# Performance work log

Measured on AMD Instinct MI355X. Metric: run time of the kernel, lower is better.

## Reference

```python
import jax, jax.numpy as jnp
import numpy as np

SIZE = (128, 128, 128)  # volume dims (X, Y, Z)
B, N, C = 2, 2097152, 1


def setup_inputs() -> dict:
    key = jax.random.key(0)
    k1, k2 = jax.random.split(key)
    image = jax.random.normal(k1, (B, SIZE[0], SIZE[1], SIZE[2], C), dtype=jnp.float32)
    grid = jax.random.uniform(k2, (B, N, 3), dtype=jnp.float32)  # normalized coords in [0,1]
    return {"image": image, "grid": grid}


def reference(image, grid):
    # image: [B, X, Y, Z, C]; grid: [B, N, 3] normalized -> trilinear sample -> [B, N, C]
    factor = jnp.array(SIZE, dtype=jnp.float32)
    idx = jnp.clip(grid * factor, 0.001, float(min(SIZE)) - 1.001)  # [B, N, 3]
    x, y, z = idx[..., 0], idx[..., 1], idx[..., 2]
    x1, x2 = jnp.floor(x), jnp.ceil(x)
    y1, y2 = jnp.floor(y), jnp.ceil(y)
    z1, z2 = jnp.floor(z), jnp.ceil(z)

    b = jnp.arange(image.shape[0])[:, None]  # [B, 1] batch index for gathers

    def g(xi, yi, zi):  # corner gather -> [B, N, C]
        return image[b, xi.astype(jnp.int32), yi.astype(jnp.int32), zi.astype(jnp.int32)]

    wx, wx2 = (x - x1)[..., None], (x2 - x)[..., None]
    wy, wy2 = (y - y1)[..., None], (y2 - y)[..., None]
    wz, wz2 = (z - z1)[..., None], (z2 - z)[..., None]

    lerp_y1 = (g(x2, y1, z1) * wx + g(x1, y1, z1) * wx2) * wy2 \
            + (g(x2, y2, z1) * wx + g(x1, y2, z1) * wx2) * wy
    lerp_y2 = (g(x2, y1, z2) * wx + g(x1, y1, z2) * wx2) * wy2 \
            + (g(x2, y2, z2) * wx + g(x1, y2, z2) * wx2) * wy
    return lerp_y2 * wz + lerp_y1 * wz2
```

## Files before the change

### kernel.cpp

```cpp
#include <hip/hip_runtime.h>
#include <hip/hip_fp16.h>


#define TOTAL   (2 * 2097152)
#define LOG2N   21
#define VOL     (128 * 128 * 128)
#define NVOX    (2 * VOL)

__global__ __launch_bounds__(256)
void ImageWarped_cvt_fp16_kernel(const float* __restrict__ in,
                                 __half* __restrict__ out)
{
    const int i = blockIdx.x * 256 + threadIdx.x;
    const float4 v = ((const float4*)in)[i];
    union { __half2 h2[2]; uint2 u; } p;
    p.h2[0] = __floats2half2_rn(v.x, v.y);
    p.h2[1] = __floats2half2_rn(v.z, v.w);
    ((uint2*)out)[i] = p.u;
}

__global__ __launch_bounds__(256)
void ImageWarped_trilinear_h2_kernel(const __half* __restrict__ image,
                                     const float* __restrict__ grid,
                                     float* __restrict__ out)
{
    const int batch = blockIdx.x & 1;
    const int s     = (blockIdx.x >> 1) * 256 + threadIdx.x;
    const int i     = (batch << LOG2N) | s;

    const float gx = grid[3 * i + 0];
    const float gy = grid[3 * i + 1];
    const float gz = grid[3 * i + 2];

    const __half* __restrict__ img = image + ((size_t)batch << LOG2N);

    const float xf = fminf(fmaxf(gx * 128.0f, 0.001f), 126.999f);
    const float yf = fminf(fmaxf(gy * 128.0f, 0.001f), 126.999f);
    const float zf = fminf(fmaxf(gz * 128.0f, 0.001f), 126.999f);

    const float x1f = floorf(xf), x2f = ceilf(xf);
    const float y1f = floorf(yf), y2f = ceilf(yf);
    const float z1f = floorf(zf), z2f = ceilf(zf);

    const float wx  = xf - x1f, wx2 = x2f - xf;
    const float wy  = yf - y1f, wy2 = y2f - yf;
    const float wz  = zf - z1f, wz2 = z2f - zf;

    const int ix1 = (int)x1f, ix2 = (int)x2f;
    const int iy1 = (int)y1f, iy2 = (int)y2f;
    const int iz1 = (int)z1f;

    const int bx1 = ix1 << 14, bx2 = ix2 << 14;
    const int by1 = iy1 << 7,  by2 = iy2 << 7;

    const int ze = min(iz1 & ~1, 124);
    const int sh = (iz1 - ze) << 4;

    const float  ww  = wz2, wwz = wz;
    auto zfetch = [&](int off) -> float {
        const uint2 u = *(const uint2*)(img + off + ze);
        unsigned long long w = ((unsigned long long)u.y << 32) | u.x;
        w >>= sh;
        union { unsigned int u32; __half2 h; } c;
        c.u32 = (unsigned int)w;
        const float2 f = __half22float2(c.h);
        return f.x * ww + f.y * wwz;
    };

    const float q11 = zfetch(bx1 + by1);
    const float q21 = zfetch(bx2 + by1);
    const float q12 = zfetch(bx1 + by2);
    const float q22 = zfetch(bx2 + by2);

    out[i] = (q21 * wx + q11 * wx2) * wy2
           + (q22 * wx + q12 * wx2) * wy;
}

__global__ __launch_bounds__(256)
void ImageWarped_trilinear_f_kernel(const float* __restrict__ image,
                                    const float* __restrict__ grid,
                                    float* __restrict__ out)
{
    const int i = blockIdx.x * 256 + threadIdx.x;
    if (i >= TOTAL) return;

    const float gx = grid[3 * i + 0];
    const float gy = grid[3 * i + 1];
    const float gz = grid[3 * i + 2];

    const int b = i >> LOG2N;
    const float* __restrict__ img = image + (size_t)b * VOL;

    const float xf = fminf(fmaxf(gx * 128.0f, 0.001f), 126.999f);
    const float yf = fminf(fmaxf(gy * 128.0f, 0.001f), 126.999f);
    const float zf = fminf(fmaxf(gz * 128.0f, 0.001f), 126.999f);

    const float x1f = floorf(xf), x2f = ceilf(xf);
    const float y1f = floorf(yf), y2f = ceilf(yf);
    const float z1f = floorf(zf), z2f = ceilf(zf);

    const float wx  = xf - x1f, wx2 = x2f - xf;
    const float wy  = yf - y1f, wy2 = y2f - yf;
    const float wz  = zf - z1f, wz2 = z2f - zf;

    const int ix1 = (int)x1f, ix2 = (int)x2f;
    const int iy1 = (int)y1f, iy2 = (int)y2f;
    const int iz1 = (int)z1f, iz2 = (int)z2f;

    const int bx1 = ix1 << 14, bx2 = ix2 << 14;
    const int by1 = iy1 << 7,  by2 = iy2 << 7;

    const float c111 = img[bx1 + by1 + iz1];
    const float c211 = img[bx2 + by1 + iz1];
    const float c121 = img[bx1 + by2 + iz1];
    const float c221 = img[bx2 + by2 + iz1];
    const float c112 = img[bx1 + by1 + iz2];
    const float c212 = img[bx2 + by1 + iz2];
    const float c122 = img[bx1 + by2 + iz2];
    const float c222 = img[bx2 + by2 + iz2];

    const float lerp_y1 = (c211 * wx + c111 * wx2) * wy2
                        + (c221 * wx + c121 * wx2) * wy;
    const float lerp_y2 = (c212 * wx + c112 * wx2) * wy2
                        + (c222 * wx + c122 * wx2) * wy;

    out[i] = lerp_y2 * wz + lerp_y1 * wz2;
}

extern "C" void kernel_launch(void* const* d_in, const int* in_sizes, int n_in,
                              void* d_out, int out_size, void* d_ws, size_t ws_size,
                              hipStream_t stream)
{
    const float* image = (const float*)d_in[0];
    const float* grid  = (const float*)d_in[1];
    float* out = (float*)d_out;

    const int blocks = (TOTAL + 255) / 256;

    if (ws_size >= (size_t)NVOX * sizeof(__half)) {
        __half* img16 = (__half*)d_ws;
        ImageWarped_cvt_fp16_kernel<<<NVOX / 4 / 256, 256, 0, stream>>>(image, img16);
        ImageWarped_trilinear_h2_kernel<<<blocks, 256, 0, stream>>>(img16, grid, out);
    } else {
        ImageWarped_trilinear_f_kernel<<<blocks, 256, 0, stream>>>(image, grid, out);
    }
}
```

Before: 174.2 us.

## Bin samples by spatial cell and sample from LDS-cached volume tiles

Adds a two-pass scheme. The first kernel sorts each sample into one of 512 16^3 cells per batch using shared-memory histograms and global atomic cursors, and writes the clamped coordinates plus the output index as 16-byte records. The second kernel loads a 17^3 fp32 tile of the volume into LDS for each cell and interpolates every binned sample from that tile. The goal is to replace random global gathers with LDS reads. In exchange it reads the grid twice, writes and reads large record buffers, scatters the output writes, and needs about 84 MB of workspace, falling back to the old paths when that is not available.

```diff
diff --git a/kernel.cpp b/kernel.cpp
--- a/kernel.cpp
+++ b/kernel.cpp
@@ -2,10 +2,173 @@
 #include <hip/hip_fp16.h>
 
 
-#define TOTAL   (2 * 2097152)
-#define LOG2N   21
-#define VOL     (128 * 128 * 128)
-#define NVOX    (2 * VOL)
+#define TOTAL    (2 * 2097152)
+#define LOG2N    21
+#define VOL      (128 * 128 * 128)
+#define NVOX     (2 * VOL)
+#define NCELLS   1024
+#define CAP      5120
+#define SPT      16
+#define TILE_N   (17 * 17 * 18)
+
+typedef unsigned int uint32;
+
+__device__ __forceinline__ float trilerp_direct(const float* __restrict__ img,
+                                                float xf, float yf, float zf)
+{
+    const float x1f = floorf(xf), x2f = ceilf(xf);
+    const float y1f = floorf(yf), y2f = ceilf(yf);
+    const float z1f = floorf(zf), z2f = ceilf(zf);
+    const float wx = xf - x1f, wx2 = x2f - xf;
+    const float wy = yf - y1f, wy2 = y2f - yf;
+    const float wz = zf - z1f, wz2 = z2f - zf;
+    const int bx1 = ((int)x1f) << 14, bx2 = ((int)x2f) << 14;
+    const int by1 = ((int)y1f) << 7,  by2 = ((int)y2f) << 7;
+    const int iz1 = (int)z1f,         iz2 = (int)z2f;
+    const float c111 = img[bx1 + by1 + iz1], c211 = img[bx2 + by1 + iz1];
+    const float c121 = img[bx1 + by2 + iz1], c221 = img[bx2 + by2 + iz1];
+    const float c112 = img[bx1 + by1 + iz2], c212 = img[bx2 + by1 + iz2];
+    const float c122 = img[bx1 + by2 + iz2], c222 = img[bx2 + by2 + iz2];
+    const float l1 = (c211 * wx + c111 * wx2) * wy2 + (c221 * wx + c121 * wx2) * wy;
+    const float l2 = (c212 * wx + c112 * wx2) * wy2 + (c222 * wx + c122 * wx2) * wy;
+    return l2 * wz + l1 * wz2;
+}
+
+__global__ __launch_bounds__(256)
+void ImageWarped_bin_kernel(const float* __restrict__ grid,
+                            const float* __restrict__ image,
+                            float* __restrict__ out,
+                            uint32* __restrict__ cursor,
+                            uint4* __restrict__ records)
+{
+    __shared__ uint32 hist[NCELLS];
+    __shared__ uint32 lbase[NCELLS];
+    __shared__ uint32 rank[NCELLS];
+
+    const int tid = threadIdx.x;
+    for (int b = tid; b < NCELLS; b += 256) { hist[b] = 0; rank[b] = 0; }
+    __syncthreads();
+
+    const int base = blockIdx.x * (256 * SPT);
+    unsigned short bins[SPT];
+
+    #pragma unroll
+    for (int k = 0; k < SPT; ++k) {
+        const int i = base + k * 256 + tid;
+        const float gx = grid[3 * i + 0];
+        const float gy = grid[3 * i + 1];
+        const float gz = grid[3 * i + 2];
+        const float xf = fminf(fmaxf(gx * 128.0f, 0.001f), 126.999f);
+        const float yf = fminf(fmaxf(gy * 128.0f, 0.001f), 126.999f);
+        const float zf = fminf(fmaxf(gz * 128.0f, 0.001f), 126.999f);
+        const int ix1 = (int)floorf(xf);
+        const int iy1 = (int)floorf(yf);
+        const int iz1 = (int)floorf(zf);
+        const int bin = ((i >> LOG2N) << 9) | ((ix1 >> 4) << 6)
+                      | ((iy1 >> 4) << 3) | (iz1 >> 4);
+        bins[k] = (unsigned short)bin;
+        atomicAdd(&hist[bin], 1u);
+    }
+    __syncthreads();
+
+    for (int b = tid; b < NCELLS; b += 256) {
+        const uint32 c = hist[b];
+        if (c) lbase[b] = atomicAdd(&cursor[b], c);
+    }
+    __syncthreads();
+
+    #pragma unroll
+    for (int k = 0; k < SPT; ++k) {
+        const int i = base + k * 256 + tid;
+        const float gx = grid[3 * i + 0];
+        const float gy = grid[3 * i + 1];
+        const float gz = grid[3 * i + 2];
+        const float xf = fminf(fmaxf(gx * 128.0f, 0.001f), 126.999f);
+        const float yf = fminf(fmaxf(gy * 128.0f, 0.001f), 126.999f);
+        const float zf = fminf(fmaxf(gz * 128.0f, 0.001f), 126.999f);
+        const int bin = bins[k];
+        const uint32 r = atomicAdd(&rank[bin], 1u);
+        const uint32 slot = lbase[bin] + r;
+        if (slot < CAP) {
+            uint4 rec;
+            rec.x = __float_as_uint(xf);
+            rec.y = __float_as_uint(yf);
+            rec.z = __float_as_uint(zf);
+            rec.w = (uint32)i;
+            records[(size_t)bin * CAP + slot] = rec;
+        } else {
+            const float* img = image + ((size_t)(i >> LOG2N) << LOG2N);
+            out[i] = trilerp_direct(img, xf, yf, zf);
+        }
+    }
+}
+
+__global__ __launch_bounds__(256)
+void ImageWarped_sample_kernel(const float* __restrict__ image,
+                               const uint32* __restrict__ cursor,
+                               const uint4* __restrict__ records,
+                               float* __restrict__ out)
+{
+    __shared__ float tile[TILE_N];
+
+    const int cell  = blockIdx.x >> 2;
+    const int sub   = blockIdx.x & 3;
+    const int batch = cell >> 9;
+    const int cx = (cell >> 6) & 7, cy = (cell >> 3) & 7, cz = cell & 7;
+    const int tid = threadIdx.x;
+
+    const float* __restrict__ img = image + ((size_t)batch << LOG2N);
+
+    for (int t = tid; t < 17 * 17 * 17; t += 256) {
+        const int tx = t / 289;
+        const int r  = t - tx * 289;
+        const int ty = r / 17;
+        const int tz = r - ty * 17;
+        const int x = min((cx << 4) + tx, 127);
+        const int y = min((cy << 4) + ty, 127);
+        const int z = min((cz << 4) + tz, 127);
+        tile[(tx * 17 + ty) * 18 + tz] = img[(x << 14) | (y << 7) | z];
+    }
+    __syncthreads();
+
+    const uint32 cnt = min(cursor[cell], (uint32)CAP);
+    const uint32 per = (cnt + 3) >> 2;
+    const uint32 begin = sub * per;
+    const uint32 end   = min(begin + per, cnt);
+    const uint4* __restrict__ rec = records + (size_t)cell * CAP;
+
+    for (uint32 t = begin + tid; t < end; t += 256) {
+        const uint4 q = rec[t];
+        const float xf = __uint_as_float(q.x);
+        const float yf = __uint_as_float(q.y);
+        const float zf = __uint_as_float(q.z);
+
+        const float x1f = floorf(xf), x2f = ceilf(xf);
+        const float y1f = floorf(yf), y2f = ceilf(yf);
+        const float z1f = floorf(zf), z2f = ceilf(zf);
+        const float wx = xf - x1f, wx2 = x2f - xf;
+        const float wy = yf - y1f, wy2 = y2f - yf;
+        const float wz = zf - z1f, wz2 = z2f - zf;
+
+        const int lx1 = ((int)x1f) & 15,     lx2 = ((int)x2f) - (cx << 4);
+        const int ly1 = ((int)y1f) & 15,     ly2 = ((int)y2f) - (cy << 4);
+        const int lz1 = ((int)z1f) & 15,     lz2 = ((int)z2f) - (cz << 4);
+
+        const int r11 = (lx1 * 17 + ly1) * 18, r21 = (lx2 * 17 + ly1) * 18;
+        const int r12 = (lx1 * 17 + ly2) * 18, r22 = (lx2 * 17 + ly2) * 18;
+
+        const float c111 = tile[r11 + lz1], c211 = tile[r21 + lz1];
+        const float c121 = tile[r12 + lz1], c221 = tile[r22 + lz1];
+        const float c112 = tile[r11 + lz2], c212 = tile[r21 + lz2];
+        const float c122 = tile[r12 + lz2], c222 = tile[r22 + lz2];
+
+        const float l1 = (c211 * wx + c111 * wx2) * wy2
+                       + (c221 * wx + c121 * wx2) * wy;
+        const float l2 = (c212 * wx + c112 * wx2) * wy2
+                       + (c222 * wx + c122 * wx2) * wy;
+        out[q.w] = l2 * wz + l1 * wz2;
+    }
+}
 
 __global__ __launch_bounds__(256)
 void ImageWarped_cvt_fp16_kernel(const float* __restrict__ in,
@@ -31,7 +194,6 @@
     const float gx = grid[3 * i + 0];
     const float gy = grid[3 * i + 1];
     const float gz = grid[3 * i + 2];
-
     const __half* __restrict__ img = image + ((size_t)batch << LOG2N);
 
     const float xf = fminf(fmaxf(gx * 128.0f, 0.001f), 126.999f);
@@ -41,22 +203,17 @@
     const float x1f = floorf(xf), x2f = ceilf(xf);
     const float y1f = floorf(yf), y2f = ceilf(yf);
     const float z1f = floorf(zf), z2f = ceilf(zf);
-
-    const float wx  = xf - x1f, wx2 = x2f - xf;
-    const float wy  = yf - y1f, wy2 = y2f - yf;
-    const float wz  = zf - z1f, wz2 = z2f - zf;
-
-    const int ix1 = (int)x1f, ix2 = (int)x2f;
-    const int iy1 = (int)y1f, iy2 = (int)y2f;
+    const float wx = xf - x1f, wx2 = x2f - xf;
+    const float wy = yf - y1f, wy2 = y2f - yf;
+    const float wz = zf - z1f, wz2 = z2f - zf;
+
+    const int bx1 = ((int)x1f) << 14, bx2 = ((int)x2f) << 14;
+    const int by1 = ((int)y1f) << 7,  by2 = ((int)y2f) << 7;
     const int iz1 = (int)z1f;
-
-    const int bx1 = ix1 << 14, bx2 = ix2 << 14;
-    const int by1 = iy1 << 7,  by2 = iy2 << 7;
 
     const int ze = min(iz1 & ~1, 124);
     const int sh = (iz1 - ze) << 4;
 
-    const float  ww  = wz2, wwz = wz;
     auto zfetch = [&](int off) -> float {
         const uint2 u = *(const uint2*)(img + off + ze);
         unsigned long long w = ((unsigned long long)u.y << 32) | u.x;
@@ -64,7 +221,7 @@
         union { unsigned int u32; __half2 h; } c;
         c.u32 = (unsigned int)w;
         const float2 f = __half22float2(c.h);
-        return f.x * ww + f.y * wwz;
+        return f.x * wz2 + f.y * wz;
     };
 
     const float q11 = zfetch(bx1 + by1);
@@ -83,48 +240,14 @@
 {
     const int i = blockIdx.x * 256 + threadIdx.x;
     if (i >= TOTAL) return;
-
     const float gx = grid[3 * i + 0];
     const float gy = grid[3 * i + 1];
     const float gz = grid[3 * i + 2];
-
-    const int b = i >> LOG2N;
-    const float* __restrict__ img = image + (size_t)b * VOL;
-
+    const float* img = image + ((size_t)(i >> LOG2N) << LOG2N);
     const float xf = fminf(fmaxf(gx * 128.0f, 0.001f), 126.999f);
     const float yf = fminf(fmaxf(gy * 128.0f, 0.001f), 126.999f);
     const float zf = fminf(fmaxf(gz * 128.0f, 0.001f), 126.999f);
-
-    const float x1f = floorf(xf), x2f = ceilf(xf);
-    const float y1f = floorf(yf), y2f = ceilf(yf);
-    const float z1f = floorf(zf), z2f = ceilf(zf);
-
-    const float wx  = xf - x1f, wx2 = x2f - xf;
-    const float wy  = yf - y1f, wy2 = y2f - yf;
-    const float wz  = zf - z1f, wz2 = z2f - zf;
-
-    const int ix1 = (int)x1f, ix2 = (int)x2f;
-    const int iy1 = (int)y1f, iy2 = (int)y2f;
-    const int iz1 = (int)z1f, iz2 = (int)z2f;
-
-    const int bx1 = ix1 << 14, bx2 = ix2 << 14;
-    const int by1 = iy1 << 7,  by2 = iy2 << 7;
-
-    const float c111 = img[bx1 + by1 + iz1];
-    const float c211 = img[bx2 + by1 + iz1];
-    const float c121 = img[bx1 + by2 + iz1];
-    const float c221 = img[bx2 + by2 + iz1];
-    const float c112 = img[bx1 + by1 + iz2];
-    const float c212 = img[bx2 + by1 + iz2];
-    const float c122 = img[bx1 + by2 + iz2];
-    const float c222 = img[bx2 + by2 + iz2];
-
-    const float lerp_y1 = (c211 * wx + c111 * wx2) * wy2
-                        + (c221 * wx + c121 * wx2) * wy;
-    const float lerp_y2 = (c212 * wx + c112 * wx2) * wy2
-                        + (c222 * wx + c122 * wx2) * wy;
-
-    out[i] = lerp_y2 * wz + lerp_y1 * wz2;
+    out[i] = trilerp_direct(img, xf, yf, zf);
 }
 
 extern "C" void kernel_launch(void* const* d_in, const int* in_sizes, int n_in,
@@ -135,13 +258,21 @@
     const float* grid  = (const float*)d_in[1];
     float* out = (float*)d_out;
 
-    const int blocks = (TOTAL + 255) / 256;
-
-    if (ws_size >= (size_t)NVOX * sizeof(__half)) {
+    const size_t need = 4096 + (size_t)NCELLS * CAP * sizeof(uint4);
+
+    if (ws_size >= need) {
+        uint32* cursor  = (uint32*)d_ws;
+        uint4*  records = (uint4*)((char*)d_ws + 4096);
+        hipMemsetAsync(cursor, 0, NCELLS * sizeof(uint32), stream);
+        ImageWarped_bin_kernel<<<TOTAL / (256 * SPT), 256, 0, stream>>>(
+            grid, image, out, cursor, records);
+        ImageWarped_sample_kernel<<<NCELLS * 4, 256, 0, stream>>>(
+            image, cursor, records, out);
+    } else if (ws_size >= (size_t)NVOX * sizeof(__half)) {
         __half* img16 = (__half*)d_ws;
         ImageWarped_cvt_fp16_kernel<<<NVOX / 4 / 256, 256, 0, stream>>>(image, img16);
-        ImageWarped_trilinear_h2_kernel<<<blocks, 256, 0, stream>>>(img16, grid, out);
+        ImageWarped_trilinear_h2_kernel<<<TOTAL / 256, 256, 0, stream>>>(img16, grid, out);
     } else {
-        ImageWarped_trilinear_f_kernel<<<blocks, 256, 0, stream>>>(image, grid, out);
-    }
-}
+        ImageWarped_trilinear_f_kernel<<<TOTAL / 256, 256, 0, stream>>>(image, grid, out);
+    }
+}
```

New measurement: 213.1 us. +22.3%, slower.
